# Performance work log

Measured on AMD Instinct MI355X. Metric: run time of the kernel, lower is better.

Reference implementation:

```python
import jax, jax.numpy as jnp
import numpy as np

# init constants: mul_vals=[1565,1342], shift_vals=[8,8]; module adds +7 to shifts
M0 = 1565
M1 = 1342
S0 = 8 + 7  # 15
S1 = 8 + 7  # 15


def _requant(x, m, s):
    # x * m, add rounding offset 1<<(s-1), truncate-to-int (torch LongTensor cast
    # truncates toward zero, matching astype on these positive-rounded values),
    # arithmetic right shift by s, clamp to [0, 255], back to float32.
    y = x * jnp.float32(m)
    y = (y + jnp.float32(1 << (s - 1))).astype(jnp.int64)
    y = jnp.right_shift(y, s).astype(jnp.float32)
    return jnp.clip(y, 0.0, 255.0)


def setup_inputs() -> dict:
    key = jax.random.key(0)
    k1, k2, k3, k4, k5 = jax.random.split(key, 5)
    B = 1048576
    X = jax.random.normal(k1, (B, 117), dtype=jnp.float32)
    W1 = jax.random.normal(k2, (20, 117), dtype=jnp.float32) * 0.1
    b1 = jax.random.normal(k3, (20,), dtype=jnp.float32) * 0.1
    W2 = jax.random.normal(k4, (2, 20), dtype=jnp.float32) * 0.1
    b2 = jax.random.normal(k5, (2,), dtype=jnp.float32) * 0.1
    return {"X": X, "W1": W1, "b1": b1, "W2": W2, "b2": b2}


def reference(X, W1, b1, W2, b2):
    # linear1: [B,117] @ [117,20] + b1
    h = jnp.einsum("bi,oi->bo", X, W1) + b1
    h = _requant(h, M0, S0)  # quantized ReLU-like clamp to [0,255]
    # linear2: [B,20] @ [20,2] + b2
    o = jnp.einsum("bi,oi->bo", h, W2) + b2
    o = _requant(o, M1, S1)
    return o
```

## Files before the change

kernel.cpp:

```cpp
#include <hip/hip_runtime.h>

#define COLS 117
#define NOUT1 20
#define ROWS 64
#define NV (ROWS * COLS / 4)
#define REM (NV - 7 * 256)
#define PSTR 21
#define PFROW (ROWS * PSTR)

__device__ __forceinline__ float requant(float x, float m, float off, int s) {
  float y = __fmul_rn(x, m);
  y = __fadd_rn(y, off);
  long long yi = (long long)y;
  yi >>= s;
  float r = (float)yi;
  return fminf(fmaxf(r, 0.0f), 255.0f);
}

__global__ void transpose_w1(const float* __restrict__ W1, float* __restrict__ w1t) {
  for (int idx = threadIdx.x; idx < NOUT1 * COLS; idx += blockDim.x) {
    int o = idx / COLS, k = idx % COLS;
    w1t[k * NOUT1 + o] = W1[idx];
  }
}

template <bool TW>
__global__ __launch_bounds__(256, 5) void fann_kernel(
    const float* __restrict__ X, const float* __restrict__ W1,
    const float* __restrict__ b1, const float* __restrict__ W2,
    const float* __restrict__ b2, float* __restrict__ out) {
  __shared__ __align__(16) float xs[ROWS * COLS];
  float4* xs4 = (float4*)xs;
  const int t = threadIdx.x;
  {
    const float4* __restrict__ src =
        reinterpret_cast<const float4*>(X + (size_t)blockIdx.x * (ROWS * COLS));
    #pragma unroll
    for (int i = 0; i < 7; ++i) xs4[t + i * 256] = src[t + i * 256];
    if (t < REM) xs4[t + 7 * 256] = src[t + 7 * 256];
  }
  __syncthreads();

  const int w = __builtin_amdgcn_readfirstlane(t >> 6);
  const int l = t & 63;
  const int k0 = w * 29;
  const int kn = (w == 3) ? 30 : 29;

  float acc[NOUT1];
  #pragma unroll
  for (int o = 0; o < NOUT1; ++o) acc[o] = 0.0f;
  const float* xr = xs + l * COLS + k0;

  if (TW) {
    const float4* __restrict__ w4 =
        reinterpret_cast<const float4*>(W1) + (size_t)k0 * (NOUT1 / 4);
    for (int kk = 0; kk < kn; ++kk) {
      float x = xr[kk];
      #pragma unroll
      for (int j = 0; j < 5; ++j) {
        float4 wv = w4[kk * 5 + j];
        acc[4 * j + 0] = fmaf(x, wv.x, acc[4 * j + 0]);
        acc[4 * j + 1] = fmaf(x, wv.y, acc[4 * j + 1]);
        acc[4 * j + 2] = fmaf(x, wv.z, acc[4 * j + 2]);
        acc[4 * j + 3] = fmaf(x, wv.w, acc[4 * j + 3]);
      }
    }
  } else {
    for (int kk = 0; kk < kn; ++kk) {
      float x = xr[kk];
      #pragma unroll
      for (int o = 0; o < NOUT1; ++o)
        acc[o] = fmaf(x, W1[o * COLS + k0 + kk], acc[o]);
    }
  }
  __syncthreads();

  {
    float* pw = xs + w * PFROW + l * PSTR;
    #pragma unroll
    for (int o = 0; o < NOUT1; ++o) pw[o] = acc[o];
  }
  __syncthreads();

  if (t < ROWS) {
    float g0[2] = {0.f, 0.f}, g1[2] = {0.f, 0.f};
    float g2[2] = {0.f, 0.f}, g3[2] = {0.f, 0.f};
    #pragma unroll
    for (int o = 0; o < NOUT1; ++o) {
      float h = xs[0 * PFROW + t * PSTR + o] + xs[1 * PFROW + t * PSTR + o] +
                xs[2 * PFROW + t * PSTR + o] + xs[3 * PFROW + t * PSTR + o];
      h += b1[o];
      float hq = requant(h, 1565.0f, 16384.0f, 15);
      float* g = (o < 5) ? g0 : (o < 10) ? g1 : (o < 15) ? g2 : g3;
      g[0] = fmaf(hq, W2[o], g[0]);
      g[1] = fmaf(hq, W2[NOUT1 + o], g[1]);
    }
    float s0 = g0[0] + g1[0] + g2[0] + g3[0] + b2[0];
    float s1 = g0[1] + g1[1] + g2[1] + g3[1] + b2[1];
    float2 r;
    r.x = requant(s0, 1342.0f, 16384.0f, 15);
    r.y = requant(s1, 1342.0f, 16384.0f, 15);
    reinterpret_cast<float2*>(out)[(size_t)blockIdx.x * ROWS + t] = r;
  }
}

__global__ void fann_tail(const float* __restrict__ X, const float* __restrict__ W1,
                          const float* __restrict__ b1, const float* __restrict__ W2,
                          const float* __restrict__ b2, float* __restrict__ out,
                          int start, int B) {
  int row = start + blockIdx.x * blockDim.x + threadIdx.x;
  if (row >= B) return;
  float acc[NOUT1];
  #pragma unroll
  for (int o = 0; o < NOUT1; ++o) acc[o] = b1[o];
  const float* xr = X + (size_t)row * COLS;
  for (int k = 0; k < COLS; ++k) {
    float x = xr[k];
    #pragma unroll
    for (int o = 0; o < NOUT1; ++o) acc[o] = fmaf(x, W1[o * COLS + k], acc[o]);
  }
  float s0 = b2[0], s1 = b2[1];
  #pragma unroll
  for (int o = 0; o < NOUT1; ++o) {
    float hq = requant(acc[o], 1565.0f, 16384.0f, 15);
    s0 = fmaf(hq, W2[o], s0);
    s1 = fmaf(hq, W2[NOUT1 + o], s1);
  }
  out[(size_t)row * 2 + 0] = requant(s0, 1342.0f, 16384.0f, 15);
  out[(size_t)row * 2 + 1] = requant(s1, 1342.0f, 16384.0f, 15);
}

extern "C" void kernel_launch(void* const* d_in, const int* in_sizes, int n_in,
                              void* d_out, int out_size, void* d_ws, size_t ws_size,
                              hipStream_t stream) {
  const float* X  = (const float*)d_in[0];
  const float* W1 = (const float*)d_in[1];
  const float* b1 = (const float*)d_in[2];
  const float* W2 = (const float*)d_in[3];
  const float* b2 = (const float*)d_in[4];
  float* out = (float*)d_out;
  const int B = in_sizes[0] / COLS;
  const int nblk = B / ROWS;
  const int tail = B - nblk * ROWS;

  const bool useT = ws_size >= (size_t)(COLS * NOUT1 * sizeof(float));
  if (useT) {
    float* w1t = (float*)d_ws;
    transpose_w1<<<1, 256, 0, stream>>>(W1, w1t);
    if (nblk > 0)
      fann_kernel<true><<<nblk, 256, 0, stream>>>(X, w1t, b1, W2, b2, out);
  } else {
    if (nblk > 0)
      fann_kernel<false><<<nblk, 256, 0, stream>>>(X, W1, b1, W2, b2, out);
  }
  if (tail > 0)
    fann_tail<<<(tail + 63) / 64, 64, 0, stream>>>(X, W1, b1, W2, b2, out,
                                                   nblk * ROWS, B);
}
```

Baseline: 117.5 us.

## Load X tiles directly into LDS and parallelize the epilogue across all waves

The global-to-register-to-LDS copy of each X tile is replaced with direct global_load_lds intrinsics, which avoid the VGPR staging and the separate LDS store instructions. The second-layer epilogue, previously run by only 64 threads, is now spread over all 256 threads. Each group of 16 lanes handles 5 hidden outputs for 16 rows, and the partial sums are combined with cross-lane shuffles. This reduces the serial tail after the GEMV, at the cost of extra shuffle work and a possible LDS layout or alignment hazard with the direct-to-LDS loads.

New measurement: 110.7 us. 1.06x faster.

```diff
diff --git a/kernel.cpp b/kernel.cpp
--- a/kernel.cpp
+++ b/kernel.cpp
@@ -34,10 +34,16 @@
   const int t = threadIdx.x;
   {
     const float4* __restrict__ src =
-        reinterpret_cast<const float4*>(X + (size_t)blockIdx.x * (ROWS * COLS));
+        reinterpret_cast<const float4*>(X) + (size_t)blockIdx.x * NV;
     #pragma unroll
-    for (int i = 0; i < 7; ++i) xs4[t + i * 256] = src[t + i * 256];
-    if (t < REM) xs4[t + 7 * 256] = src[t + 7 * 256];
+    for (int i = 0; i < 7; ++i)
+      __builtin_amdgcn_global_load_lds(
+          (const __attribute__((address_space(1))) void*)&src[t + i * 256],
+          (__attribute__((address_space(3))) void*)&xs4[t + i * 256], 16, 0, 0);
+    if (t < REM)
+      __builtin_amdgcn_global_load_lds(
+          (const __attribute__((address_space(1))) void*)&src[t + 7 * 256],
+          (__attribute__((address_space(3))) void*)&xs4[t + 7 * 256], 16, 0, 0);
   }
   __syncthreads();
 
@@ -82,25 +88,35 @@
   }
   __syncthreads();
 
-  if (t < ROWS) {
-    float g0[2] = {0.f, 0.f}, g1[2] = {0.f, 0.f};
-    float g2[2] = {0.f, 0.f}, g3[2] = {0.f, 0.f};
+  {
+    const int r  = (w << 4) + (l & 15);
+    const int og = l >> 4;
+    float g0 = 0.0f, g1 = 0.0f;
     #pragma unroll
-    for (int o = 0; o < NOUT1; ++o) {
-      float h = xs[0 * PFROW + t * PSTR + o] + xs[1 * PFROW + t * PSTR + o] +
-                xs[2 * PFROW + t * PSTR + o] + xs[3 * PFROW + t * PSTR + o];
+    for (int j = 0; j < 5; ++j) {
+      const int o = og * 5 + j;
+      const float* pa = xs + r * PSTR + o;
+      float h = pa[0 * PFROW] + pa[1 * PFROW] + pa[2 * PFROW] + pa[3 * PFROW];
       h += b1[o];
       float hq = requant(h, 1565.0f, 16384.0f, 15);
-      float* g = (o < 5) ? g0 : (o < 10) ? g1 : (o < 15) ? g2 : g3;
-      g[0] = fmaf(hq, W2[o], g[0]);
-      g[1] = fmaf(hq, W2[NOUT1 + o], g[1]);
+      g0 = fmaf(hq, W2[o], g0);
+      g1 = fmaf(hq, W2[NOUT1 + o], g1);
     }
-    float s0 = g0[0] + g1[0] + g2[0] + g3[0] + b2[0];
-    float s1 = g0[1] + g1[1] + g2[1] + g3[1] + b2[1];
-    float2 r;
-    r.x = requant(s0, 1342.0f, 16384.0f, 15);
-    r.y = requant(s1, 1342.0f, 16384.0f, 15);
-    reinterpret_cast<float2*>(out)[(size_t)blockIdx.x * ROWS + t] = r;
+    const int lb = l & 15;
+    float a01 = __shfl(g0, lb + 16);
+    float a02 = __shfl(g0, lb + 32);
+    float a03 = __shfl(g0, lb + 48);
+    float a11 = __shfl(g1, lb + 16);
+    float a12 = __shfl(g1, lb + 32);
+    float a13 = __shfl(g1, lb + 48);
+    if (og == 0) {
+      float s0 = ((g0 + a01) + a02) + a03 + b2[0];
+      float s1 = ((g1 + a11) + a12) + a13 + b2[1];
+      float2 res;
+      res.x = requant(s0, 1342.0f, 16384.0f, 15);
+      res.y = requant(s1, 1342.0f, 16384.0f, 15);
+      reinterpret_cast<float2*>(out)[(size_t)blockIdx.x * ROWS + r] = res;
+    }
   }
 }
 
```
